# Performance work log

Measured on AMD Instinct MI355X. Metric: run time of the kernel, lower is better.

## Reference

```python
import jax, jax.numpy as jnp
import numpy as np

NUM_NODES = 50000
NUM_EDGES = 800000
NUM_GRAPHS = 256
FEAT = 128
STATE = 64
ROUNDS = 4
M = 32


def setup_inputs() -> dict:
    key = jax.random.key(0)
    ks = jax.random.split(key, 12)
    x = jax.random.normal(ks[0], (NUM_NODES, FEAT), dtype=jnp.float32)
    edge_index = jax.random.randint(ks[1], (2, NUM_EDGES), 0, NUM_NODES, dtype=jnp.int64)
    batch = jnp.sort(jax.random.randint(ks[2], (NUM_NODES,), 0, NUM_GRAPHS, dtype=jnp.int64))
    s = 0.1  # weight init scale
    return {
        "x": x,
        "edge_index": edge_index,
        "batch": batch,
        "in_W": jax.random.normal(ks[3], (FEAT, STATE), dtype=jnp.float32) * s,
        "in_b": jnp.zeros((STATE,), dtype=jnp.float32),
        "msg_W": jax.random.normal(ks[4], (ROUNDS, STATE, STATE), dtype=jnp.float32) * s,
        "msg_b": jnp.zeros((ROUNDS, STATE), dtype=jnp.float32),
        "upd_W": jax.random.normal(ks[5], (ROUNDS, STATE, STATE), dtype=jnp.float32) * s,
        "upd_b": jnp.zeros((ROUNDS, STATE), dtype=jnp.float32),
        "mean_W": jax.random.normal(ks[6], (STATE, M), dtype=jnp.float32) * s,
        "mean_b": jnp.zeros((M,), dtype=jnp.float32),
        "logvar_W": jax.random.normal(ks[7], (STATE, M), dtype=jnp.float32) * s,
        "logvar_b": jnp.zeros((M,), dtype=jnp.float32),
    }


def reference(x, edge_index, batch, in_W, in_b, msg_W, msg_b, upd_W, upd_b,
              mean_W, mean_b, logvar_W, logvar_b):
    num_nodes = x.shape[0]
    src, dst = edge_index[0], edge_index[1]  # (to, from) -> gather src, scatter dst
    # input net (dropout is identity in eval mode)
    state = jax.nn.relu(x @ in_W + in_b)  # [N, S]
    for r in range(ROUNDS):
        message = jax.nn.relu(state @ msg_W[r] + msg_b[r])          # [N, S]
        gathered = message[src]                                       # [E, S] irregular gather
        aggregated = jax.ops.segment_sum(gathered, dst, num_segments=num_nodes)  # [N, S] scatter-add
        state = state + jax.nn.relu(aggregated @ upd_W[r] + upd_b[r])
    graph_state = jax.ops.segment_sum(state, batch, num_segments=NUM_GRAPHS)  # [G, S]
    mean = graph_state @ mean_W + mean_b                              # [G, M]
    log_var = jnp.clip(graph_state @ logvar_W + logvar_b, -20.0, 2.0)
    std = jnp.exp(0.5 * log_var)
    return jnp.stack([mean, std])  # [2, G, M] -> Normal(mean, std) params
```

## Files before the change

kernel.cpp:

```cpp
#include <hip/hip_runtime.h>
#include <math.h>

#define NODES  50000
#define EDGES  800000
#define GRAPHS 256
#define FEAT   128
#define STATE  64
#define M_OUT  32
#define ROUNDS 4
#define NT32   ((NODES + 31) / 32)
#define CAP    64
#define OVFMAX 8192

typedef unsigned short bfraw;

__device__ __forceinline__ bfraw f2bf(float f) {
    union { float f; unsigned int i; } v; v.f = f;
    unsigned int r = v.i + 0x7FFF + ((v.i >> 16) & 1);
    return (bfraw)(r >> 16);
}
__device__ __forceinline__ int packbf(float lo, float hi) {
    return ((int)f2bf(hi) << 16) | (int)f2bf(lo);
}
__device__ __forceinline__ void addv8(float* acc, int4 v, float m) {
    union { int i; float f; } t;
    t.i = v.x << 16;                  acc[0] += t.f * m;
    t.i = v.x & (int)0xffff0000;      acc[1] += t.f * m;
    t.i = v.y << 16;                  acc[2] += t.f * m;
    t.i = v.y & (int)0xffff0000;      acc[3] += t.f * m;
    t.i = v.z << 16;                  acc[4] += t.f * m;
    t.i = v.z & (int)0xffff0000;      acc[5] += t.f * m;
    t.i = v.w << 16;                  acc[6] += t.f * m;
    t.i = v.w & (int)0xffff0000;      acc[7] += t.f * m;
}
__device__ __forceinline__ int4 pack8(const float* a) {
    int4 o;
    o.x = packbf(a[0], a[1]); o.y = packbf(a[2], a[3]);
    o.z = packbf(a[4], a[5]); o.w = packbf(a[6], a[7]);
    return o;
}

__global__ __launch_bounds__(256) void k_fill(
    const int* __restrict__ ei, int* __restrict__ cnt,
    unsigned short* __restrict__ csr, int* __restrict__ ovfc, int* __restrict__ ovf)
{
    int e = blockIdx.x * 256 + threadIdx.x;
    if (e >= EDGES) return;
    int src = __builtin_nontemporal_load(ei + e);
    int dst = __builtin_nontemporal_load(ei + EDGES + e);
    int slot = atomicAdd(&cnt[dst], 1);
    if (slot < CAP) csr[(long)dst * CAP + slot] = (unsigned short)src;
    else { int o = atomicAdd(ovfc, 1); if (o < OVFMAX) ovf[o] = (dst << 16) | src; }
}

__device__ __forceinline__ void gather_to_lds(
    const int* __restrict__ cnt, const unsigned short* __restrict__ csr,
    const int* __restrict__ ovfc, const int* __restrict__ ovf,
    const bfraw* __restrict__ msg, float* __restrict__ sa)
{
    float dummy = 0.f;
    {
        long s = (long)blockIdx.x * 2048 + (long)threadIdx.x * 8;
        if (s + 8 <= (long)NODES * STATE) {
            int4 a = *(const int4*)(msg + s);
            union { int i; float f; } t; t.i = a.x << 16;
            dummy = t.f;
        }
    }

    const int row = threadIdx.x >> 3;
    const int q   = (threadIdx.x & 7) * 8;
    const int n   = blockIdx.x * 32 + row;

    int cn = (n < NODES) ? cnt[n] : 0;
    if (cn > CAP) cn = CAP;
    const unsigned short* crow = csr + (long)n * CAP;

    float acc[8] = {0.f, 0.f, 0.f, 0.f, 0.f, 0.f, 0.f, 0.f};
    for (int i = 0; i < cn; i += 8) {
        int4 ia = *(const int4*)(crow + i);
        int rem = cn - i;
        int idx[8];
        idx[0] = ia.x & 0xffff; idx[1] = ((unsigned)ia.x) >> 16;
        idx[2] = ia.y & 0xffff; idx[3] = ((unsigned)ia.y) >> 16;
        idx[4] = ia.z & 0xffff; idx[5] = ((unsigned)ia.z) >> 16;
        idx[6] = ia.w & 0xffff; idx[7] = ((unsigned)ia.w) >> 16;
        int4 v[8];
        #pragma unroll
        for (int j = 0; j < 8; j++) {
            int s_ = (j < rem) ? idx[j] : idx[0];
            v[j] = *(const int4*)(msg + (long)s_ * STATE + q);
        }
        #pragma unroll
        for (int j = 0; j < 8; j++) addv8(acc, v[j], (j < rem) ? 1.f : 0.f);
    }
    acc[0] += dummy * 0.0f;

    int oc = *ovfc;
    if (oc > 0) {
        if (oc > OVFMAX) oc = OVFMAX;
        for (int t = 0; t < oc; t++) {
            int pk = ovf[t];
            if ((pk >> 16) == n) {
                int4 v = *(const int4*)(msg + (long)(pk & 0xffff) * STATE + q);
                addv8(acc, v, 1.f);
            }
        }
    }

    *(float4*)(sa + row * 68 + q)     = make_float4(acc[0], acc[1], acc[2], acc[3]);
    *(float4*)(sa + row * 68 + q + 4) = make_float4(acc[4], acc[5], acc[6], acc[7]);
}

__global__ __launch_bounds__(256) void k_in_msg(
    const float* __restrict__ x, const float* __restrict__ inW, const float* __restrict__ inb,
    const float* __restrict__ msgW, const float* __restrict__ msgb,
    float* __restrict__ state, bfraw* __restrict__ msg)
{
    __shared__ float sW[64 * STATE];
    __shared__ float sB[32 * 68];
    __shared__ float sInb[STATE], sMsgb[STATE];

    const int row = threadIdx.x >> 3;
    const int q8  = (threadIdx.x & 7) << 3;
    const int base = blockIdx.x * 32;
    const int n = base + row;

    if (threadIdx.x < STATE) {
        sInb[threadIdx.x]  = inb[threadIdx.x];
        sMsgb[threadIdx.x] = msgb[threadIdx.x];
    }
    for (int i = threadIdx.x; i < 512; i += 256) {
        int r = i >> 4, q = (i & 15) << 2;
        float4 v = make_float4(0.f, 0.f, 0.f, 0.f);
        if (base + r < NODES) v = *(const float4*)(x + (long)(base + r) * FEAT + q);
        *(float4*)(sB + r * 68 + q) = v;
    }
    for (int i = threadIdx.x; i < 1024; i += 256)
        *(float4*)(sW + i * 4) = *(const float4*)(inW + i * 4);
    __syncthreads();

    float a[8];
    #pragma unroll
    for (int j = 0; j < 8; j++) a[j] = sInb[q8 + j];
    const float* xr = sB + row * 68;
    #pragma unroll 8
    for (int k = 0; k < 64; k++) {
        float xv = xr[k];
        float4 w0 = *(const float4*)(sW + k * STATE + q8);
        float4 w1 = *(const float4*)(sW + k * STATE + q8 + 4);
        a[0] += xv * w0.x; a[1] += xv * w0.y; a[2] += xv * w0.z; a[3] += xv * w0.w;
        a[4] += xv * w1.x; a[5] += xv * w1.y; a[6] += xv * w1.z; a[7] += xv * w1.w;
    }
    __syncthreads();
    for (int i = threadIdx.x; i < 512; i += 256) {
        int r = i >> 4, q = (i & 15) << 2;
        float4 v = make_float4(0.f, 0.f, 0.f, 0.f);
        if (base + r < NODES) v = *(const float4*)(x + (long)(base + r) * FEAT + 64 + q);
        *(float4*)(sB + r * 68 + q) = v;
    }
    for (int i = threadIdx.x; i < 1024; i += 256)
        *(float4*)(sW + i * 4) = *(const float4*)(inW + 64 * STATE + i * 4);
    __syncthreads();
    #pragma unroll 8
    for (int k = 0; k < 64; k++) {
        float xv = xr[k];
        float4 w0 = *(const float4*)(sW + k * STATE + q8);
        float4 w1 = *(const float4*)(sW + k * STATE + q8 + 4);
        a[0] += xv * w0.x; a[1] += xv * w0.y; a[2] += xv * w0.z; a[3] += xv * w0.w;
        a[4] += xv * w1.x; a[5] += xv * w1.y; a[6] += xv * w1.z; a[7] += xv * w1.w;
    }
    #pragma unroll
    for (int j = 0; j < 8; j++) a[j] = fmaxf(a[j], 0.f);
    if (n < NODES) {
        *(float4*)(state + (long)n * STATE + q8)     = make_float4(a[0], a[1], a[2], a[3]);
        *(float4*)(state + (long)n * STATE + q8 + 4) = make_float4(a[4], a[5], a[6], a[7]);
    }
    __syncthreads();
    *(float4*)(sB + row * 68 + q8)     = make_float4(a[0], a[1], a[2], a[3]);
    *(float4*)(sB + row * 68 + q8 + 4) = make_float4(a[4], a[5], a[6], a[7]);
    for (int i = threadIdx.x; i < 1024; i += 256)
        *(float4*)(sW + i * 4) = *(const float4*)(msgW + i * 4);
    __syncthreads();

    float m[8];
    #pragma unroll
    for (int j = 0; j < 8; j++) m[j] = sMsgb[q8 + j];
    const float* sr = sB + row * 68;
    #pragma unroll 8
    for (int k = 0; k < STATE; k++) {
        float sv = sr[k];
        float4 w0 = *(const float4*)(sW + k * STATE + q8);
        float4 w1 = *(const float4*)(sW + k * STATE + q8 + 4);
        m[0] += sv * w0.x; m[1] += sv * w0.y; m[2] += sv * w0.z; m[3] += sv * w0.w;
        m[4] += sv * w1.x; m[5] += sv * w1.y; m[6] += sv * w1.z; m[7] += sv * w1.w;
    }
    #pragma unroll
    for (int j = 0; j < 8; j++) m[j] = fmaxf(m[j], 0.f);
    if (n < NODES)
        *(int4*)(msg + (long)n * STATE + q8) = pack8(m);
}

__global__ __launch_bounds__(256) void k_round_msg(
    const int* __restrict__ cnt, const unsigned short* __restrict__ csr,
    const int* __restrict__ ovfc, const int* __restrict__ ovf,
    const bfraw* __restrict__ msg_in,
    const float* __restrict__ updW, const float* __restrict__ updb,
    const float* __restrict__ msgW, const float* __restrict__ msgb,
    float* __restrict__ state, bfraw* __restrict__ msg_out)
{
    __shared__ float sW[64 * STATE];
    __shared__ float sUpdb[STATE], sMsgb[STATE];
    __shared__ float sa[32 * 68];

    const int row = threadIdx.x >> 3;
    const int q8  = (threadIdx.x & 7) << 3;
    const int n = blockIdx.x * 32 + row;

    if (threadIdx.x < STATE) {
        sUpdb[threadIdx.x] = updb[threadIdx.x];
        sMsgb[threadIdx.x] = msgb[threadIdx.x];
    }
    for (int i = threadIdx.x; i < 1024; i += 256)
        *(float4*)(sW + i * 4) = *(const float4*)(updW + i * 4);

    gather_to_lds(cnt, csr, ovfc, ovf, msg_in, sa);
    __syncthreads();

    float a[8];
    #pragma unroll
    for (int j = 0; j < 8; j++) a[j] = sUpdb[q8 + j];
    const float* ar = sa + row * 68;
    #pragma unroll 8
    for (int k = 0; k < STATE; k++) {
        float av = ar[k];
        float4 w0 = *(const float4*)(sW + k * STATE + q8);
        float4 w1 = *(const float4*)(sW + k * STATE + q8 + 4);
        a[0] += av * w0.x; a[1] += av * w0.y; a[2] += av * w0.z; a[3] += av * w0.w;
        a[4] += av * w1.x; a[5] += av * w1.y; a[6] += av * w1.z; a[7] += av * w1.w;
    }
    #pragma unroll
    for (int j = 0; j < 8; j++) a[j] = fmaxf(a[j], 0.f);
    float s[8] = {0.f,0.f,0.f,0.f,0.f,0.f,0.f,0.f};
    if (n < NODES) {
        float4 st0 = *(const float4*)(state + (long)n * STATE + q8);
        float4 st1 = *(const float4*)(state + (long)n * STATE + q8 + 4);
        s[0] = st0.x + a[0]; s[1] = st0.y + a[1]; s[2] = st0.z + a[2]; s[3] = st0.w + a[3];
        s[4] = st1.x + a[4]; s[5] = st1.y + a[5]; s[6] = st1.z + a[6]; s[7] = st1.w + a[7];
        *(float4*)(state + (long)n * STATE + q8)     = make_float4(s[0], s[1], s[2], s[3]);
        *(float4*)(state + (long)n * STATE + q8 + 4) = make_float4(s[4], s[5], s[6], s[7]);
    }
    __syncthreads();
    *(float4*)(sa + row * 68 + q8)     = make_float4(s[0], s[1], s[2], s[3]);
    *(float4*)(sa + row * 68 + q8 + 4) = make_float4(s[4], s[5], s[6], s[7]);
    for (int i = threadIdx.x; i < 1024; i += 256)
        *(float4*)(sW + i * 4) = *(const float4*)(msgW + i * 4);
    __syncthreads();

    float m[8];
    #pragma unroll
    for (int j = 0; j < 8; j++) m[j] = sMsgb[q8 + j];
    const float* sr = sa + row * 68;
    #pragma unroll 8
    for (int k = 0; k < STATE; k++) {
        float sv = sr[k];
        float4 w0 = *(const float4*)(sW + k * STATE + q8);
        float4 w1 = *(const float4*)(sW + k * STATE + q8 + 4);
        m[0] += sv * w0.x; m[1] += sv * w0.y; m[2] += sv * w0.z; m[3] += sv * w0.w;
        m[4] += sv * w1.x; m[5] += sv * w1.y; m[6] += sv * w1.z; m[7] += sv * w1.w;
    }
    #pragma unroll
    for (int j = 0; j < 8; j++) m[j] = fmaxf(m[j], 0.f);
    if (n < NODES)
        *(int4*)(msg_out + (long)n * STATE + q8) = pack8(m);
}

__global__ __launch_bounds__(256) void k_round_pool(
    const int* __restrict__ cnt, const unsigned short* __restrict__ csr,
    const int* __restrict__ ovfc, const int* __restrict__ ovf,
    const bfraw* __restrict__ msg_in,
    const float* __restrict__ updW, const float* __restrict__ updb,
    const float* __restrict__ state, const int* __restrict__ batch,
    float* __restrict__ gs)
{
    __shared__ float sW[64 * STATE];
    __shared__ float sUpdb[STATE];
    __shared__ float sa[32 * 68];
    __shared__ int   sg[32];

    const int row = threadIdx.x >> 3;
    const int q8  = (threadIdx.x & 7) << 3;
    const int base = blockIdx.x * 32;
    const int n = base + row;

    if (threadIdx.x < STATE) sUpdb[threadIdx.x] = updb[threadIdx.x];
    for (int i = threadIdx.x; i < 1024; i += 256)
        *(float4*)(sW + i * 4) = *(const float4*)(updW + i * 4);
    if (threadIdx.x < 32) {
        int nn = base + threadIdx.x;
        sg[threadIdx.x] = batch[nn < NODES ? nn : NODES - 1];
    }

    gather_to_lds(cnt, csr, ovfc, ovf, msg_in, sa);
    __syncthreads();

    float a[8];
    #pragma unroll
    for (int j = 0; j < 8; j++) a[j] = sUpdb[q8 + j];
    const float* ar = sa + row * 68;
    #pragma unroll 8
    for (int k = 0; k < STATE; k++) {
        float av = ar[k];
        float4 w0 = *(const float4*)(sW + k * STATE + q8);
        float4 w1 = *(const float4*)(sW + k * STATE + q8 + 4);
        a[0] += av * w0.x; a[1] += av * w0.y; a[2] += av * w0.z; a[3] += av * w0.w;
        a[4] += av * w1.x; a[5] += av * w1.y; a[6] += av * w1.z; a[7] += av * w1.w;
    }
    float s[8] = {0.f,0.f,0.f,0.f,0.f,0.f,0.f,0.f};
    if (n < NODES) {
        float4 st0 = *(const float4*)(state + (long)n * STATE + q8);
        float4 st1 = *(const float4*)(state + (long)n * STATE + q8 + 4);
        s[0] = st0.x + fmaxf(a[0], 0.f); s[1] = st0.y + fmaxf(a[1], 0.f);
        s[2] = st0.z + fmaxf(a[2], 0.f); s[3] = st0.w + fmaxf(a[3], 0.f);
        s[4] = st1.x + fmaxf(a[4], 0.f); s[5] = st1.y + fmaxf(a[5], 0.f);
        s[6] = st1.z + fmaxf(a[6], 0.f); s[7] = st1.w + fmaxf(a[7], 0.f);
    }
    __syncthreads();
    *(float4*)(sa + row * 68 + q8)     = make_float4(s[0], s[1], s[2], s[3]);
    *(float4*)(sa + row * 68 + q8 + 4) = make_float4(s[4], s[5], s[6], s[7]);
    __syncthreads();

    if (threadIdx.x < STATE) {
        const int f = threadIdx.x;
        float run = sa[f];
        int g = sg[0];
        #pragma unroll
        for (int r = 1; r < 32; r++) {
            int g2 = sg[r];
            float v = sa[r * 68 + f];
            if (g2 != g) {
                atomicAdd(&gs[g * STATE + f], run);
                run = v; g = g2;
            } else {
                run += v;
            }
        }
        atomicAdd(&gs[g * STATE + f], run);
    }
}

__global__ __launch_bounds__(64) void k_final(
    const float* __restrict__ gs,
    const float* __restrict__ meanW, const float* __restrict__ meanb,
    const float* __restrict__ lvW, const float* __restrict__ lvb,
    float* __restrict__ out)
{
    __shared__ float row[STATE];
    const int g = blockIdx.x;
    const int j = threadIdx.x;
    row[j] = gs[g * STATE + j];
    __syncthreads();
    if (j < M_OUT) {
        float acc = meanb[j];
        #pragma unroll
        for (int k = 0; k < STATE; k++) acc += row[k] * meanW[k * M_OUT + j];
        out[g * M_OUT + j] = acc;
    } else {
        int jj = j - M_OUT;
        float acc = lvb[jj];
        #pragma unroll
        for (int k = 0; k < STATE; k++) acc += row[k] * lvW[k * M_OUT + jj];
        acc = fminf(fmaxf(acc, -20.f), 2.f);
        out[GRAPHS * M_OUT + g * M_OUT + jj] = expf(0.5f * acc);
    }
}

extern "C" void kernel_launch(void* const* d_in, const int* in_sizes, int n_in,
                              void* d_out, int out_size, void* d_ws, size_t ws_size,
                              hipStream_t stream) {
    const float* x     = (const float*)d_in[0];
    const int*   ei    = (const int*)d_in[1];
    const int*   batch = (const int*)d_in[2];
    const float* inW   = (const float*)d_in[3];
    const float* inb   = (const float*)d_in[4];
    const float* msgW  = (const float*)d_in[5];
    const float* msgb  = (const float*)d_in[6];
    const float* updW  = (const float*)d_in[7];
    const float* updb  = (const float*)d_in[8];
    const float* meanW = (const float*)d_in[9];
    const float* meanb = (const float*)d_in[10];
    const float* lvW   = (const float*)d_in[11];
    const float* lvb   = (const float*)d_in[12];
    float* out = (float*)d_out;

    const size_t NS   = (size_t)NODES * STATE * sizeof(float);
    const size_t MSGB = (size_t)NODES * STATE * sizeof(bfraw);
    char* ws = (char*)d_ws;
    size_t off = 0;
    auto alloc = [&](size_t bytes) { void* p = ws + off; off += (bytes + 255) & ~(size_t)255; return p; };
    float* state  = (float*)alloc(NS);
    bfraw* msgA   = (bfraw*)alloc(MSGB);
    bfraw* msgB   = (bfraw*)alloc(MSGB);
    float* gs     = (float*)alloc((size_t)GRAPHS * STATE * sizeof(float));
    int*   cnt    = (int*)alloc((size_t)NODES * sizeof(int));
    int*   ovfc   = (int*)alloc(256);
    int*   ovf    = (int*)alloc((size_t)OVFMAX * sizeof(int));
    unsigned short* csr = (unsigned short*)alloc((size_t)NODES * CAP * sizeof(unsigned short));

    hipMemsetAsync(cnt, 0, (size_t)NODES * sizeof(int), stream);
    hipMemsetAsync(ovfc, 0, sizeof(int), stream);
    hipMemsetAsync(gs, 0, (size_t)GRAPHS * STATE * sizeof(float), stream);

    k_fill<<<(EDGES + 255) / 256, 256, 0, stream>>>(ei, cnt, csr, ovfc, ovf);
    k_in_msg<<<NT32, 256, 0, stream>>>(x, inW, inb, msgW, msgb, state, msgA);

    bfraw *mi = msgA, *mo = msgB;
    for (int r = 0; r < ROUNDS; r++) {
        if (r < ROUNDS - 1) {
            k_round_msg<<<NT32, 256, 0, stream>>>(
                cnt, csr, ovfc, ovf, mi,
                updW + r * STATE * STATE, updb + r * STATE,
                msgW + (r + 1) * STATE * STATE, msgb + (r + 1) * STATE,
                state, mo);
            bfraw* t = mi; mi = mo; mo = t;
        } else {
            k_round_pool<<<NT32, 256, 0, stream>>>(
                cnt, csr, ovfc, ovf, mi,
                updW + r * STATE * STATE, updb + r * STATE,
                state, batch, gs);
        }
    }

    k_final<<<GRAPHS, 64, 0, stream>>>(gs, meanW, meanb, lvW, lvb, out);
}
```

Before: 309.3 us.

## Split message gather into two feature-half planes with separate kernels

The message tensor is stored as two column-half planes of 32 features each, so each gather pass works over a 3.2 MB bf16 table that fits better in cache. Gathering moves out of the fused round kernels into a dedicated kernel that stages CSR rows in LDS and writes a bf16 aggregate buffer. The update kernels then read that aggregate back. This trades two extra launches per round and an aggregate round-trip through memory, at bf16 precision, for better cache hit rates on the random gathers.

```diff
diff --git a/kernel.cpp b/kernel.cpp
--- a/kernel.cpp
+++ b/kernel.cpp
@@ -9,7 +9,10 @@
 #define M_OUT  32
 #define ROUNDS 4
 #define NT32   ((NODES + 31) / 32)
+#define NT64   ((NODES + 63) / 64)
+#define HALF   32
 #define CAP    64
+#define CROW   72
 #define OVFMAX 8192
 
 typedef unsigned short bfraw;
@@ -33,6 +36,17 @@
     t.i = v.w << 16;                  acc[6] += t.f * m;
     t.i = v.w & (int)0xffff0000;      acc[7] += t.f * m;
 }
+__device__ __forceinline__ void unpack8(float* d, int4 v) {
+    union { int i; float f; } t;
+    t.i = v.x << 16;              d[0] = t.f;
+    t.i = v.x & (int)0xffff0000;  d[1] = t.f;
+    t.i = v.y << 16;              d[2] = t.f;
+    t.i = v.y & (int)0xffff0000;  d[3] = t.f;
+    t.i = v.z << 16;              d[4] = t.f;
+    t.i = v.z & (int)0xffff0000;  d[5] = t.f;
+    t.i = v.w << 16;              d[6] = t.f;
+    t.i = v.w & (int)0xffff0000;  d[7] = t.f;
+}
 __device__ __forceinline__ int4 pack8(const float* a) {
     int4 o;
     o.x = packbf(a[0], a[1]); o.y = packbf(a[2], a[3]);
@@ -53,28 +67,43 @@
     else { int o = atomicAdd(ovfc, 1); if (o < OVFMAX) ovf[o] = (dst << 16) | src; }
 }
 
-__device__ __forceinline__ void gather_to_lds(
+__global__ __launch_bounds__(256) void k_gather_half(
     const int* __restrict__ cnt, const unsigned short* __restrict__ csr,
     const int* __restrict__ ovfc, const int* __restrict__ ovf,
-    const bfraw* __restrict__ msg, float* __restrict__ sa)
-{
+    const bfraw* __restrict__ plane,
+    bfraw* __restrict__ agg, int halfsel)
+{
+    __shared__ unsigned short sCsr[64 * CROW];
+    __shared__ int sCnt[64];
+
+    const int base = blockIdx.x * 64;
+
+    for (int i = threadIdx.x; i < 512; i += 256) {
+        int r = i >> 3;
+        int c = (i & 7) << 3;
+        long rr = base + r; if (rr >= NODES) rr = NODES - 1;
+        *(int4*)(sCsr + r * CROW + c) = *(const int4*)(csr + rr * CAP + c);
+    }
+    if (threadIdx.x < 64) {
+        int nn = base + threadIdx.x;
+        sCnt[threadIdx.x] = (nn < NODES) ? cnt[nn] : 0;
+    }
     float dummy = 0.f;
     {
         long s = (long)blockIdx.x * 2048 + (long)threadIdx.x * 8;
-        if (s + 8 <= (long)NODES * STATE) {
-            int4 a = *(const int4*)(msg + s);
+        if (s + 8 <= (long)NODES * HALF) {
+            int4 a = *(const int4*)(plane + s);
             union { int i; float f; } t; t.i = a.x << 16;
             dummy = t.f;
         }
     }
-
-    const int row = threadIdx.x >> 3;
-    const int q   = (threadIdx.x & 7) * 8;
-    const int n   = blockIdx.x * 32 + row;
-
-    int cn = (n < NODES) ? cnt[n] : 0;
-    if (cn > CAP) cn = CAP;
-    const unsigned short* crow = csr + (long)n * CAP;
+    __syncthreads();
+
+    const int row  = threadIdx.x >> 2;
+    const int q    = (threadIdx.x & 3) * 8;
+    const int n    = base + row;
+    int cn = sCnt[row]; if (cn > CAP) cn = CAP;
+    const unsigned short* crow = sCsr + row * CROW;
 
     float acc[8] = {0.f, 0.f, 0.f, 0.f, 0.f, 0.f, 0.f, 0.f};
     for (int i = 0; i < cn; i += 8) {
@@ -89,7 +118,7 @@
         #pragma unroll
         for (int j = 0; j < 8; j++) {
             int s_ = (j < rem) ? idx[j] : idx[0];
-            v[j] = *(const int4*)(msg + (long)s_ * STATE + q);
+            v[j] = *(const int4*)(plane + (long)s_ * HALF + q);
         }
         #pragma unroll
         for (int j = 0; j < 8; j++) addv8(acc, v[j], (j < rem) ? 1.f : 0.f);
@@ -102,20 +131,20 @@
         for (int t = 0; t < oc; t++) {
             int pk = ovf[t];
             if ((pk >> 16) == n) {
-                int4 v = *(const int4*)(msg + (long)(pk & 0xffff) * STATE + q);
+                int4 v = *(const int4*)(plane + (long)(pk & 0xffff) * HALF + q);
                 addv8(acc, v, 1.f);
             }
         }
     }
 
-    *(float4*)(sa + row * 68 + q)     = make_float4(acc[0], acc[1], acc[2], acc[3]);
-    *(float4*)(sa + row * 68 + q + 4) = make_float4(acc[4], acc[5], acc[6], acc[7]);
+    if (n < NODES)
+        *(int4*)(agg + (long)n * STATE + halfsel * HALF + q) = pack8(acc);
 }
 
 __global__ __launch_bounds__(256) void k_in_msg(
     const float* __restrict__ x, const float* __restrict__ inW, const float* __restrict__ inb,
     const float* __restrict__ msgW, const float* __restrict__ msgb,
-    float* __restrict__ state, bfraw* __restrict__ msg)
+    float* __restrict__ state, bfraw* __restrict__ msg0, bfraw* __restrict__ msg1)
 {
     __shared__ float sW[64 * STATE];
     __shared__ float sB[32 * 68];
@@ -197,17 +226,17 @@
     }
     #pragma unroll
     for (int j = 0; j < 8; j++) m[j] = fmaxf(m[j], 0.f);
-    if (n < NODES)
-        *(int4*)(msg + (long)n * STATE + q8) = pack8(m);
-}
-
-__global__ __launch_bounds__(256) void k_round_msg(
-    const int* __restrict__ cnt, const unsigned short* __restrict__ csr,
-    const int* __restrict__ ovfc, const int* __restrict__ ovf,
-    const bfraw* __restrict__ msg_in,
+    if (n < NODES) {
+        bfraw* dst = (q8 < HALF) ? (msg0 + (long)n * HALF + q8) : (msg1 + (long)n * HALF + (q8 - HALF));
+        *(int4*)dst = pack8(m);
+    }
+}
+
+__global__ __launch_bounds__(256) void k_upd_msg(
+    const bfraw* __restrict__ agg,
     const float* __restrict__ updW, const float* __restrict__ updb,
     const float* __restrict__ msgW, const float* __restrict__ msgb,
-    float* __restrict__ state, bfraw* __restrict__ msg_out)
+    float* __restrict__ state, bfraw* __restrict__ msg0, bfraw* __restrict__ msg1)
 {
     __shared__ float sW[64 * STATE];
     __shared__ float sUpdb[STATE], sMsgb[STATE];
@@ -223,8 +252,12 @@
     }
     for (int i = threadIdx.x; i < 1024; i += 256)
         *(float4*)(sW + i * 4) = *(const float4*)(updW + i * 4);
-
-    gather_to_lds(cnt, csr, ovfc, ovf, msg_in, sa);
+    {
+        float tmp[8] = {0.f,0.f,0.f,0.f,0.f,0.f,0.f,0.f};
+        if (n < NODES) unpack8(tmp, *(const int4*)(agg + (long)n * STATE + q8));
+        *(float4*)(sa + row * 68 + q8)     = make_float4(tmp[0], tmp[1], tmp[2], tmp[3]);
+        *(float4*)(sa + row * 68 + q8 + 4) = make_float4(tmp[4], tmp[5], tmp[6], tmp[7]);
+    }
     __syncthreads();
 
     float a[8];
@@ -271,14 +304,14 @@
     }
     #pragma unroll
     for (int j = 0; j < 8; j++) m[j] = fmaxf(m[j], 0.f);
-    if (n < NODES)
-        *(int4*)(msg_out + (long)n * STATE + q8) = pack8(m);
-}
-
-__global__ __launch_bounds__(256) void k_round_pool(
-    const int* __restrict__ cnt, const unsigned short* __restrict__ csr,
-    const int* __restrict__ ovfc, const int* __restrict__ ovf,
-    const bfraw* __restrict__ msg_in,
+    if (n < NODES) {
+        bfraw* dst = (q8 < HALF) ? (msg0 + (long)n * HALF + q8) : (msg1 + (long)n * HALF + (q8 - HALF));
+        *(int4*)dst = pack8(m);
+    }
+}
+
+__global__ __launch_bounds__(256) void k_upd_pool(
+    const bfraw* __restrict__ agg,
     const float* __restrict__ updW, const float* __restrict__ updb,
     const float* __restrict__ state, const int* __restrict__ batch,
     float* __restrict__ gs)
@@ -296,12 +329,16 @@
     if (threadIdx.x < STATE) sUpdb[threadIdx.x] = updb[threadIdx.x];
     for (int i = threadIdx.x; i < 1024; i += 256)
         *(float4*)(sW + i * 4) = *(const float4*)(updW + i * 4);
+    {
+        float tmp[8] = {0.f,0.f,0.f,0.f,0.f,0.f,0.f,0.f};
+        if (n < NODES) unpack8(tmp, *(const int4*)(agg + (long)n * STATE + q8));
+        *(float4*)(sa + row * 68 + q8)     = make_float4(tmp[0], tmp[1], tmp[2], tmp[3]);
+        *(float4*)(sa + row * 68 + q8 + 4) = make_float4(tmp[4], tmp[5], tmp[6], tmp[7]);
+    }
     if (threadIdx.x < 32) {
         int nn = base + threadIdx.x;
         sg[threadIdx.x] = batch[nn < NODES ? nn : NODES - 1];
     }
-
-    gather_to_lds(cnt, csr, ovfc, ovf, msg_in, sa);
     __syncthreads();
 
     float a[8];
@@ -394,13 +431,17 @@
     float* out = (float*)d_out;
 
     const size_t NS   = (size_t)NODES * STATE * sizeof(float);
-    const size_t MSGB = (size_t)NODES * STATE * sizeof(bfraw);
+    const size_t PLB  = (size_t)NODES * HALF * sizeof(bfraw);
+    const size_t AGB  = (size_t)NODES * STATE * sizeof(bfraw);
     char* ws = (char*)d_ws;
     size_t off = 0;
     auto alloc = [&](size_t bytes) { void* p = ws + off; off += (bytes + 255) & ~(size_t)255; return p; };
     float* state  = (float*)alloc(NS);
-    bfraw* msgA   = (bfraw*)alloc(MSGB);
-    bfraw* msgB   = (bfraw*)alloc(MSGB);
+    bfraw* msgA0  = (bfraw*)alloc(PLB);
+    bfraw* msgA1  = (bfraw*)alloc(PLB);
+    bfraw* msgB0  = (bfraw*)alloc(PLB);
+    bfraw* msgB1  = (bfraw*)alloc(PLB);
+    bfraw* agg    = (bfraw*)alloc(AGB);
     float* gs     = (float*)alloc((size_t)GRAPHS * STATE * sizeof(float));
     int*   cnt    = (int*)alloc((size_t)NODES * sizeof(int));
     int*   ovfc   = (int*)alloc(256);
@@ -412,20 +453,23 @@
     hipMemsetAsync(gs, 0, (size_t)GRAPHS * STATE * sizeof(float), stream);
 
     k_fill<<<(EDGES + 255) / 256, 256, 0, stream>>>(ei, cnt, csr, ovfc, ovf);
-    k_in_msg<<<NT32, 256, 0, stream>>>(x, inW, inb, msgW, msgb, state, msgA);
-
-    bfraw *mi = msgA, *mo = msgB;
+    k_in_msg<<<NT32, 256, 0, stream>>>(x, inW, inb, msgW, msgb, state, msgA0, msgA1);
+
+    bfraw *mi0 = msgA0, *mi1 = msgA1, *mo0 = msgB0, *mo1 = msgB1;
     for (int r = 0; r < ROUNDS; r++) {
+        k_gather_half<<<NT64, 256, 0, stream>>>(cnt, csr, ovfc, ovf, mi0, agg, 0);
+        k_gather_half<<<NT64, 256, 0, stream>>>(cnt, csr, ovfc, ovf, mi1, agg, 1);
         if (r < ROUNDS - 1) {
-            k_round_msg<<<NT32, 256, 0, stream>>>(
-                cnt, csr, ovfc, ovf, mi,
+            k_upd_msg<<<NT32, 256, 0, stream>>>(
+                agg,
                 updW + r * STATE * STATE, updb + r * STATE,
                 msgW + (r + 1) * STATE * STATE, msgb + (r + 1) * STATE,
-                state, mo);
-            bfraw* t = mi; mi = mo; mo = t;
+                state, mo0, mo1);
+            bfraw* t0 = mi0; mi0 = mo0; mo0 = t0;
+            bfraw* t1 = mi1; mi1 = mo1; mo1 = t1;
         } else {
-            k_round_pool<<<NT32, 256, 0, stream>>>(
-                cnt, csr, ovfc, ovf, mi,
+            k_upd_pool<<<NT32, 256, 0, stream>>>(
+                agg,
                 updW + r * STATE * STATE, updb + r * STATE,
                 state, batch, gs);
         }
```

Measured after the change: 377.7 us. 22.1% more time.
